# Kernel tuning notes

Hardware: AMD Instinct MI355X
Metric: run time of the kernel (lower is better)

Reference implementation:

```python
import jax, jax.numpy as jnp
import numpy as np

ROPE_BASE = 10000.0


def _rope_tables(T, d, dtype):
    # inv_freq over even indices, emb = concat(freqs, freqs) -> [T, d]
    inv_freq = 1.0 / (ROPE_BASE ** (jnp.arange(0, d, 2, dtype=jnp.float32) / d))
    t = jnp.arange(T, dtype=jnp.float32)
    freqs = jnp.einsum('i,j->ij', t, inv_freq)          # [T, d/2]
    emb = jnp.concatenate([freqs, freqs], axis=-1)      # [T, d]
    return jnp.cos(emb).astype(dtype), jnp.sin(emb).astype(dtype)


def _rotate_half(x):
    d = x.shape[-1] // 2
    return jnp.concatenate([-x[..., d:], x[..., :d]], axis=-1)


def _apply_rope(x, cos, sin):
    # x: [B, T, H, Dh]; cos/sin: [T, Dh] broadcast over batch and heads
    c = cos[None, :, None, :]
    s = sin[None, :, None, :]
    return x * c + _rotate_half(x) * s


def setup_inputs() -> dict:
    key = jax.random.key(0)
    k1, k2, k3 = jax.random.split(key, 3)
    B, T, C = 2, 2048, 1024
    x = jax.random.normal(k1, (B, T, C), dtype=jnp.float32)
    # weights stored as [in, out] (transposed nn.Linear), scaled like torch init
    W_qkv = jax.random.normal(k2, (C, 3 * C), dtype=jnp.float32) * (C ** -0.5)
    W_proj = jax.random.normal(k3, (C, C), dtype=jnp.float32) * (C ** -0.5)
    return {'x': x, 'W_qkv': W_qkv, 'W_proj': W_proj}


def reference(x, W_qkv, W_proj):
    B, T, C = x.shape
    H = 16
    Dh = C // H
    qkv = x @ W_qkv                                   # [B, T, 3C]
    q, k, v = jnp.split(qkv, 3, axis=-1)
    q = q.reshape(B, T, H, Dh)
    k = k.reshape(B, T, H, Dh)
    v = v.reshape(B, T, H, Dh)
    cos, sin = _rope_tables(T, Dh, x.dtype)
    q = _apply_rope(q, cos, sin)
    k = _apply_rope(k, cos, sin)
    scale = 1.0 / jnp.sqrt(jnp.asarray(Dh, dtype=x.dtype))
    # causal SDPA: scores [B, H, T, T]
    scores = jnp.einsum('bqhd,bkhd->bhqk', q, k) * scale
    causal = jnp.tril(jnp.ones((T, T), dtype=bool))
    scores = jnp.where(causal[None, None], scores, jnp.asarray(-jnp.inf, dtype=scores.dtype))
    attn = jax.nn.softmax(scores, axis=-1)
    y = jnp.einsum('bhqk,bkhd->bqhd', attn, v).reshape(B, T, C)
    return y @ W_proj
```

## Files before the change

kernel.cpp:

```cpp
#include <hip/hip_runtime.h>
#include <cstdint>
#include <cstddef>

typedef __bf16 bf16;
typedef __bf16 bf16x2 __attribute__((ext_vector_type(2)));
typedef __bf16 bf16x4 __attribute__((ext_vector_type(4)));
typedef __bf16 bf16x8 __attribute__((ext_vector_type(8)));
typedef float  f32x4  __attribute__((ext_vector_type(4)));
typedef float  f32x16 __attribute__((ext_vector_type(16)));
typedef int    i32x4  __attribute__((ext_vector_type(4)));

#define G2L(src, dst)                                                          \
  __builtin_amdgcn_global_load_lds(                                            \
      (const __attribute__((address_space(1))) unsigned int*)(src),            \
      (__attribute__((address_space(3))) unsigned int*)(dst), 16, 0, 0)

__global__ void k_f32_to_bf16(const float* __restrict__ in, bf16* __restrict__ out, int n) {
  int i = (blockIdx.x * blockDim.x + threadIdx.x) * 8;
  if (i >= n) return;
  float4 a = *(const float4*)(in + i);
  float4 b = *(const float4*)(in + i + 4);
  bf16x8 o;
  o[0] = (bf16)a.x; o[1] = (bf16)a.y; o[2] = (bf16)a.z; o[3] = (bf16)a.w;
  o[4] = (bf16)b.x; o[5] = (bf16)b.y; o[6] = (bf16)b.z; o[7] = (bf16)b.w;
  *(bf16x8*)(out + i) = o;
}

__global__ void k_transpose_f32_bf16(const float* __restrict__ in, bf16* __restrict__ out,
                                     int R, int C) {
  __shared__ float tile[32][33];
  int c0 = blockIdx.x * 32, r0 = blockIdx.y * 32;
  int tx = threadIdx.x & 31, ty = threadIdx.x >> 5;
#pragma unroll
  for (int i = 0; i < 32; i += 8)
    tile[ty + i][tx] = in[(size_t)(r0 + ty + i) * C + c0 + tx];
  __syncthreads();
#pragma unroll
  for (int i = 0; i < 32; i += 8)
    out[(size_t)(c0 + ty + i) * R + r0 + tx] = (bf16)tile[tx][ty + i];
}

__global__ void k_rope_tables(float* __restrict__ cosT, float* __restrict__ sinT, int total) {
  int i = blockIdx.x * blockDim.x + threadIdx.x;
  if (i >= total) return;
  int t = i >> 5, j = i & 31;
  float inv = powf(10000.0f, -(float)j * (1.0f / 32.0f));
  float f = (float)t * inv;
  cosT[i] = cosf(f);
  sinT[i] = sinf(f);
}

__global__ void k_rope_qk(const bf16* __restrict__ qkv, const float* __restrict__ cosT,
                          const float* __restrict__ sinT, bf16* __restrict__ qr,
                          bf16* __restrict__ kr) {
  int i = blockIdx.x * blockDim.x + threadIdx.x;
  int j = i & 31;
  int h = (i >> 5) & 15;
  int t = (i >> 9) & 2047;
  int b = i >> 20;
  size_t base = (size_t)(b * 2048 + t) * 3072;
  float c = cosT[t * 32 + j], s = sinT[t * 32 + j];
  float qlo = (float)qkv[base + h * 64 + j];
  float qhi = (float)qkv[base + h * 64 + j + 32];
  float klo = (float)qkv[base + 1024 + h * 64 + j];
  float khi = (float)qkv[base + 1024 + h * 64 + j + 32];
  size_t ob = ((size_t)(b * 16 + h) * 2048 + t) * 64;
  qr[ob + j]      = (bf16)((qlo * c - qhi * s) * 0.125f);
  qr[ob + j + 32] = (bf16)((qhi * c + qlo * s) * 0.125f);
  kr[ob + j]      = (bf16)(klo * c - khi * s);
  kr[ob + j + 32] = (bf16)(khi * c + klo * s);
}

__global__ void k_v_scatter(const bf16* __restrict__ qkv, bf16* __restrict__ vt) {
  __shared__ bf16 tile[64][66];
  int bh = blockIdx.y;
  int t0 = blockIdx.x * 64;
  int b = bh >> 4, h = bh & 15;
  int tt = threadIdx.x >> 2, c4 = (threadIdx.x & 3) * 16;
  const bf16* src = qkv + (size_t)(b * 2048 + t0 + tt) * 3072 + 2048 + h * 64 + c4;
  bf16x8 v0 = *(const bf16x8*)src;
  bf16x8 v1 = *(const bf16x8*)(src + 8);
#pragma unroll
  for (int j = 0; j < 8; j++) { tile[tt][c4 + j] = v0[j]; tile[tt][c4 + 8 + j] = v1[j]; }
  __syncthreads();
  int d = threadIdx.x >> 2, tc0 = (threadIdx.x & 3) * 16;
  bf16x8 o0, o1;
#pragma unroll
  for (int j = 0; j < 8; j++) { o0[j] = tile[tc0 + j][d]; o1[j] = tile[tc0 + 8 + j][d]; }
  bf16* dst = vt + ((size_t)bh * 64 + d) * 2048 + t0 + tc0;
  *(bf16x8*)dst = o0;
  *(bf16x8*)(dst + 8) = o1;
}

template <int OUTF32>
__global__ __launch_bounds__(256) void k_gemm_bt(const bf16* __restrict__ A,
                                                 const bf16* __restrict__ Bt,
                                                 float* __restrict__ Cf, bf16* __restrict__ Cb,
                                                 int M, int N, int K) {
  __shared__ __align__(16) bf16 sA[128 * 64];
  __shared__ __align__(16) bf16 sB[128 * 64];
  int m0 = blockIdx.y * 128, n0 = blockIdx.x * 128;
  int t = threadIdx.x, lane = t & 63, w = t >> 6;
  int wr = w >> 1, wc = w & 1;
  int lr = lane & 15, q2 = lane >> 4;
  int srow8 = lane >> 3, pc8 = lane & 7;
  f32x4 acc[4][4] = {};
  for (int k0 = 0; k0 < K; k0 += 64) {
#pragma unroll
    for (int is = 0; is < 4; is++) {
      int r = w * 32 + is * 8 + srow8;
      int lc = pc8 ^ (r & 7);
      G2L(A + (size_t)(m0 + r) * K + k0 + lc * 8, &sA[(w * 32 + is * 8) * 64]);
    }
#pragma unroll
    for (int is = 0; is < 4; is++) {
      int r = w * 32 + is * 8 + srow8;
      int lc = pc8 ^ (r & 7);
      G2L(Bt + (size_t)(n0 + r) * K + k0 + lc * 8, &sB[(w * 32 + is * 8) * 64]);
    }
    __syncthreads();
#pragma unroll
    for (int ch = 0; ch < 2; ch++) {
      bf16x8 af[4], bfr[4];
#pragma unroll
      for (int i = 0; i < 4; i++) {
        int r = wr * 64 + i * 16 + lr;
        af[i] = *(const bf16x8*)&sA[r * 64 + (((ch * 4 + q2) ^ (r & 7)) * 8)];
      }
#pragma unroll
      for (int i = 0; i < 4; i++) {
        int r = wc * 64 + i * 16 + lr;
        bfr[i] = *(const bf16x8*)&sB[r * 64 + (((ch * 4 + q2) ^ (r & 7)) * 8)];
      }
#pragma unroll
      for (int mi = 0; mi < 4; mi++)
#pragma unroll
        for (int ni = 0; ni < 4; ni++)
          acc[mi][ni] = __builtin_amdgcn_mfma_f32_16x16x32_bf16(af[mi], bfr[ni], acc[mi][ni], 0, 0, 0);
    }
    __syncthreads();
  }
  int row_base = m0 + wr * 64, col_base = n0 + wc * 64;
#pragma unroll
  for (int mi = 0; mi < 4; mi++)
#pragma unroll
    for (int ni = 0; ni < 4; ni++) {
      int col = col_base + ni * 16 + lr;
#pragma unroll
      for (int r = 0; r < 4; r++) {
        int row = row_base + mi * 16 + q2 * 4 + r;
        float v = acc[mi][ni][r];
        if (OUTF32) Cf[(size_t)row * N + col] = v;
        else        Cb[(size_t)row * N + col] = (bf16)v;
      }
    }
}

__global__ __launch_bounds__(128) void k_flash(const bf16* __restrict__ qr,
                                               const bf16* __restrict__ kr,
                                               const bf16* __restrict__ vt,
                                               bf16* __restrict__ out) {
  const int T = 2048;
  int bx = blockIdx.x;
  int by = blockIdx.y;
  int qb = (by & 16) ? (31 - bx) : bx;
  int bh = by;
  int b = bh >> 4, h = bh & 15;
  __shared__ __align__(16) bf16 sK[2][64 * 64];
  __shared__ __align__(16) bf16 sV[2][64 * 64];
  int t = threadIdx.x, lane = t & 63, w = t >> 6;
  int q31 = lane & 31, hi = lane >> 5;
  int srow8 = lane >> 3, pc8 = lane & 7;

  const bf16* Kbh = kr + (size_t)bh * T * 64;
  const bf16* Vbh = vt + (size_t)bh * 64 * T;

  int nk = qb + 1;
  int qwb = qb * 64 + w * 32;
  int qg = qwb + q31;

  const bf16* qrow = qr + ((size_t)bh * T + qg) * 64 + hi * 8;
  bf16x8 qf[4];
#pragma unroll
  for (int ks = 0; ks < 4; ks++) qf[ks] = *(const bf16x8*)(qrow + ks * 16);
  f32x16 o0 = {}, o1 = {};
  float m = -1e30f, l = 0.f;

  auto stage = [&](int buf, int kt) {
#pragma unroll
    for (int is = 0; is < 4; is++) {
      int r = w * 32 + is * 8 + srow8;
      int lc = pc8 ^ (r & 7);
      G2L(Kbh + (size_t)(kt * 64 + r) * 64 + lc * 8, &sK[buf][(w * 32 + is * 8) * 64]);
    }
#pragma unroll
    for (int is = 0; is < 4; is++) {
      int d = w * 32 + is * 8 + srow8;
      int lc = pc8 ^ (d & 7);
      G2L(Vbh + (size_t)d * T + kt * 64 + lc * 8, &sV[buf][(w * 32 + is * 8) * 64]);
    }
  };

  stage(0, 0);
  for (int kt = 0; kt < nk; kt++) {
    int buf = kt & 1;
    if (kt + 1 < nk) {
      stage(buf ^ 1, kt + 1);
      asm volatile("s_waitcnt vmcnt(8)" ::: "memory");
    } else {
      asm volatile("s_waitcnt vmcnt(0)" ::: "memory");
    }
    __builtin_amdgcn_s_barrier();
    asm volatile("" ::: "memory");
    __builtin_amdgcn_sched_barrier(0);
    const bf16* Kb = &sK[buf][0];
    const bf16* Vb = &sV[buf][0];
    f32x16 s[2];
#pragma unroll
    for (int kb = 0; kb < 2; kb++) {
      f32x16 a = {};
      int krow = kb * 32 + q31;
#pragma unroll
      for (int ks = 0; ks < 4; ks++) {
        int ch = (ks * 2 + hi) ^ (krow & 7);
        bf16x8 kf = *(const bf16x8*)&Kb[krow * 64 + ch * 8];
        a = __builtin_amdgcn_mfma_f32_32x32x16_bf16(kf, qf[ks], a, 0, 0, 0);
      }
      s[kb] = a;
    }
    if (kt == qb) {
      int thr = qg - kt * 64;
#pragma unroll
      for (int kb = 0; kb < 2; kb++)
#pragma unroll
        for (int r = 0; r < 16; r++) {
          int koff = kb * 32 + (r & 3) + 8 * (r >> 2) + 4 * hi;
          if (koff > thr) s[kb][r] = -1e30f;
        }
    }
    float px = -1e30f;
#pragma unroll
    for (int kb = 0; kb < 2; kb++)
#pragma unroll
      for (int r = 0; r < 16; r++) px = fmaxf(px, s[kb][r]);
    px = fmaxf(px, __shfl_xor(px, 32, 64));
    float mn = fmaxf(m, px);
    float alpha = __expf(m - mn);
    m = mn;
    float rs = 0.f;
#pragma unroll
    for (int kb = 0; kb < 2; kb++)
#pragma unroll
      for (int r = 0; r < 16; r++) {
        float p = __expf(s[kb][r] - m);
        s[kb][r] = p;
        rs += p;
      }
    rs += __shfl_xor(rs, 32, 64);
    l = l * alpha + rs;
    int pw[4][4];
#pragma unroll
    for (int kb = 0; kb < 2; kb++) {
      int wd[8];
#pragma unroll
      for (int g = 0; g < 4; g++) {
        bf16x2 a, c;
        a[0] = (bf16)s[kb][4 * g + 0]; a[1] = (bf16)s[kb][4 * g + 1];
        c[0] = (bf16)s[kb][4 * g + 2]; c[1] = (bf16)s[kb][4 * g + 3];
        wd[2 * g]     = __builtin_bit_cast(int, a);
        wd[2 * g + 1] = __builtin_bit_cast(int, c);
      }
      asm volatile("v_permlane32_swap_b32 %0, %1" : "+v"(wd[0]), "+v"(wd[2]));
      asm volatile("v_permlane32_swap_b32 %0, %1" : "+v"(wd[1]), "+v"(wd[3]));
      asm volatile("v_permlane32_swap_b32 %0, %1" : "+v"(wd[4]), "+v"(wd[6]));
      asm volatile("v_permlane32_swap_b32 %0, %1" : "+v"(wd[5]), "+v"(wd[7]));
      pw[2 * kb][0] = wd[0]; pw[2 * kb][1] = wd[1];
      pw[2 * kb][2] = wd[2]; pw[2 * kb][3] = wd[3];
      pw[2 * kb + 1][0] = wd[4]; pw[2 * kb + 1][1] = wd[5];
      pw[2 * kb + 1][2] = wd[6]; pw[2 * kb + 1][3] = wd[7];
    }
#pragma unroll
    for (int r = 0; r < 16; r++) { o0[r] *= alpha; o1[r] *= alpha; }
#pragma unroll
    for (int ks = 0; ks < 4; ks++) {
      i32x4 pv = {pw[ks][0], pw[ks][1], pw[ks][2], pw[ks][3]};
      bf16x8 pb = __builtin_bit_cast(bf16x8, pv);
      {
        int drow = q31;
        int ch = (ks * 2 + hi) ^ (drow & 7);
        bf16x8 vf = *(const bf16x8*)&Vb[drow * 64 + ch * 8];
        o0 = __builtin_amdgcn_mfma_f32_32x32x16_bf16(vf, pb, o0, 0, 0, 0);
      }
      {
        int drow = 32 + q31;
        int ch = (ks * 2 + hi) ^ (drow & 7);
        bf16x8 vf = *(const bf16x8*)&Vb[drow * 64 + ch * 8];
        o1 = __builtin_amdgcn_mfma_f32_32x32x16_bf16(vf, pb, o1, 0, 0, 0);
      }
    }
    asm volatile("" ::: "memory");
    __builtin_amdgcn_s_barrier();
    asm volatile("" ::: "memory");
  }
  float linv = 1.0f / l;
  bf16* orow = out + ((size_t)b * T + qg) * 1024 + h * 64;
#pragma unroll
  for (int g = 0; g < 4; g++) {
    bf16x4 v0, v1;
#pragma unroll
    for (int j = 0; j < 4; j++) {
      v0[j] = (bf16)(o0[4 * g + j] * linv);
      v1[j] = (bf16)(o1[4 * g + j] * linv);
    }
    *(bf16x4*)&orow[8 * g + 4 * hi]      = v0;
    *(bf16x4*)&orow[32 + 8 * g + 4 * hi] = v1;
  }
}

extern "C" void kernel_launch(void* const* d_in, const int* in_sizes, int n_in,
                              void* d_out, int out_size, void* d_ws, size_t ws_size,
                              hipStream_t stream) {
  const float* x     = (const float*)d_in[0];
  const float* Wqkv  = (const float*)d_in[1];
  const float* Wproj = (const float*)d_in[2];
  float* outp = (float*)d_out;
  const int B = 2, T = 2048, C = 1024;
  const int M = B * T;

  char* ws = (char*)d_ws;
  size_t off = 0;
  auto alloc = [&](size_t bytes) {
    void* p = ws + off;
    off += (bytes + 255) & ~(size_t)255;
    return p;
  };
  bf16* xb     = (bf16*)alloc((size_t)M * C * 2);
  bf16* wqkvt  = (bf16*)alloc((size_t)3 * C * C * 2);
  bf16* wprojt = (bf16*)alloc((size_t)C * C * 2);
  float* cosT  = (float*)alloc((size_t)T * 32 * 4);
  float* sinT  = (float*)alloc((size_t)T * 32 * 4);
  bf16* qkv    = (bf16*)alloc((size_t)M * 3 * C * 2);
  bf16* qr     = (bf16*)alloc((size_t)M * C * 2);
  bf16* kr     = (bf16*)alloc((size_t)M * C * 2);
  bf16* vt     = (bf16*)alloc((size_t)M * C * 2);
  bf16* attn   = qkv;

  k_f32_to_bf16<<<dim3(M * C / 8 / 256), dim3(256), 0, stream>>>(x, xb, M * C);
  k_transpose_f32_bf16<<<dim3(3 * C / 32, C / 32), dim3(256), 0, stream>>>(Wqkv, wqkvt, C, 3 * C);
  k_transpose_f32_bf16<<<dim3(C / 32, C / 32), dim3(256), 0, stream>>>(Wproj, wprojt, C, C);
  k_rope_tables<<<dim3(T * 32 / 256), dim3(256), 0, stream>>>(cosT, sinT, T * 32);
  k_gemm_bt<0><<<dim3(3 * C / 128, M / 128), dim3(256), 0, stream>>>(xb, wqkvt, (float*)nullptr, qkv, M, 3 * C, C);
  k_rope_qk<<<dim3((B * T * 16 * 32) / 256), dim3(256), 0, stream>>>(qkv, cosT, sinT, qr, kr);
  k_v_scatter<<<dim3(T / 64, 32), dim3(256), 0, stream>>>(qkv, vt);
  k_flash<<<dim3(32, 32), dim3(128), 0, stream>>>(qr, kr, vt, attn);
  k_gemm_bt<1><<<dim3(C / 128, M / 128), dim3(256), 0, stream>>>(attn, wprojt, outp, (bf16*)nullptr, M, C, C);
}
```

Baseline: 150.4 us.

## Schedule flash blocks longest-first, tree-reduce softmax, raise MFMA priority

Result: faster. 140.8 us (-6.4%).

```diff
diff --git a/kernel.cpp b/kernel.cpp
--- a/kernel.cpp
+++ b/kernel.cpp
@@ -161,10 +161,9 @@
                                                const bf16* __restrict__ vt,
                                                bf16* __restrict__ out) {
   const int T = 2048;
-  int bx = blockIdx.x;
-  int by = blockIdx.y;
-  int qb = (by & 16) ? (31 - bx) : bx;
-  int bh = by;
+  int id = blockIdx.x;
+  int qb = 31 - (id >> 5);
+  int bh = id & 31;
   int b = bh >> 4, h = bh & 15;
   __shared__ __align__(16) bf16 sK[2][64 * 64];
   __shared__ __align__(16) bf16 sV[2][64 * 64];
@@ -216,6 +215,7 @@
     const bf16* Kb = &sK[buf][0];
     const bf16* Vb = &sV[buf][0];
     f32x16 s[2];
+    __builtin_amdgcn_s_setprio(1);
 #pragma unroll
     for (int kb = 0; kb < 2; kb++) {
       f32x16 a = {};
@@ -228,6 +228,7 @@
       }
       s[kb] = a;
     }
+    __builtin_amdgcn_s_setprio(0);
     if (kt == qb) {
       int thr = qg - kt * 64;
 #pragma unroll
@@ -238,24 +239,32 @@
           if (koff > thr) s[kb][r] = -1e30f;
         }
     }
-    float px = -1e30f;
-#pragma unroll
-    for (int kb = 0; kb < 2; kb++)
-#pragma unroll
-      for (int r = 0; r < 16; r++) px = fmaxf(px, s[kb][r]);
+    float tm[16];
+#pragma unroll
+    for (int i = 0; i < 16; i++) tm[i] = fmaxf(s[0][i], s[1][i]);
+#pragma unroll
+    for (int st = 8; st > 0; st >>= 1)
+#pragma unroll
+      for (int i = 0; i < st; i++) tm[i] = fmaxf(tm[i], tm[i + st]);
+    float px = tm[0];
     px = fmaxf(px, __shfl_xor(px, 32, 64));
     float mn = fmaxf(m, px);
     float alpha = __expf(m - mn);
     m = mn;
-    float rs = 0.f;
-#pragma unroll
-    for (int kb = 0; kb < 2; kb++)
-#pragma unroll
-      for (int r = 0; r < 16; r++) {
-        float p = __expf(s[kb][r] - m);
-        s[kb][r] = p;
-        rs += p;
-      }
+    float ts[16];
+#pragma unroll
+    for (int i = 0; i < 16; i++) {
+      float p0 = __expf(s[0][i] - m);
+      float p1 = __expf(s[1][i] - m);
+      s[0][i] = p0;
+      s[1][i] = p1;
+      ts[i] = p0 + p1;
+    }
+#pragma unroll
+    for (int st = 8; st > 0; st >>= 1)
+#pragma unroll
+      for (int i = 0; i < st; i++) ts[i] += ts[i + st];
+    float rs = ts[0];
     rs += __shfl_xor(rs, 32, 64);
     l = l * alpha + rs;
     int pw[4][4];
@@ -281,6 +290,7 @@
     }
 #pragma unroll
     for (int r = 0; r < 16; r++) { o0[r] *= alpha; o1[r] *= alpha; }
+    __builtin_amdgcn_s_setprio(1);
 #pragma unroll
     for (int ks = 0; ks < 4; ks++) {
       i32x4 pv = {pw[ks][0], pw[ks][1], pw[ks][2], pw[ks][3]};
@@ -298,6 +308,7 @@
         o1 = __builtin_amdgcn_mfma_f32_32x32x16_bf16(vf, pb, o1, 0, 0, 0);
       }
     }
+    __builtin_amdgcn_s_setprio(0);
     asm volatile("" ::: "memory");
     __builtin_amdgcn_s_barrier();
     asm volatile("" ::: "memory");
@@ -352,6 +363,6 @@
   k_gemm_bt<0><<<dim3(3 * C / 128, M / 128), dim3(256), 0, stream>>>(xb, wqkvt, (float*)nullptr, qkv, M, 3 * C, C);
   k_rope_qk<<<dim3((B * T * 16 * 32) / 256), dim3(256), 0, stream>>>(qkv, cosT, sinT, qr, kr);
   k_v_scatter<<<dim3(T / 64, 32), dim3(256), 0, stream>>>(qkv, vt);
-  k_flash<<<dim3(32, 32), dim3(128), 0, stream>>>(qr, kr, vt, attn);
+  k_flash<<<dim3(1024), dim3(128), 0, stream>>>(qr, kr, vt, attn);
   k_gemm_bt<1><<<dim3(C / 128, M / 128), dim3(256), 0, stream>>>(attn, wprojt, outp, (bf16*)nullptr, M, C, C);
 }
```
